# Performance work log

Measured on AMD Instinct MI355X. Metric: run time of the kernel, lower is better.

The kernel has to match this reference:

```python
import jax, jax.numpy as jnp
import numpy as np

B, T, D, E, H = 8, 2048, 1024, 8, 256
LN_EPS = 1e-5  # torch.nn.LayerNorm default


def setup_inputs() -> dict:
    key = jax.random.key(0)
    ks = jax.random.split(key, 4)
    return {
        "x": jax.random.normal(ks[0], (B, T, D), dtype=jnp.float32),
        "Wg": jax.random.normal(ks[1], (E, D), dtype=jnp.float32) * 0.02,
        "ln_scale": jnp.ones((E, D), dtype=jnp.float32),
        "ln_bias": jnp.zeros((E, D), dtype=jnp.float32),
        "W1": jax.random.normal(ks[2], (E, D, H), dtype=jnp.float32) * 0.02,
        "b1": jnp.zeros((E, H), dtype=jnp.float32),
        "W2": jax.random.normal(ks[3], (E, H, D), dtype=jnp.float32) * 0.02,
        "b2": jnp.zeros((E, D), dtype=jnp.float32),
    }


def reference(x, Wg, ln_scale, ln_bias, W1, b1, W2, b2):
    Bs, Ts, Ds = x.shape
    xt = x.reshape(Bs * Ts, Ds)                      # [N, D]
    logits = xt @ Wg.T                               # [N, E]
    # softmax is monotone, so argmax(softmax(logits)) == argmax(logits)
    top1 = jnp.argmax(logits, axis=-1)               # [N] int

    # LayerNorm normalization is expert-independent; compute once.
    mu = jnp.mean(xt, axis=-1, keepdims=True)
    var = jnp.mean(jnp.square(xt - mu), axis=-1, keepdims=True)
    xhat = (xt - mu) * jax.lax.rsqrt(var + LN_EPS)   # [N, D]

    n_experts = Wg.shape[0]

    def body(y, p):
        s_e, b_e, w1, bb1, w2, bb2, eid = p
        h = jax.nn.gelu((xhat * s_e + b_e) @ w1 + bb1, approximate=False)  # [N, H]
        out = h @ w2 + bb2                                                  # [N, D]
        mask = (top1 == eid)[:, None].astype(out.dtype)
        return y + mask * out, None

    y0 = jnp.zeros_like(xt)
    y, _ = jax.lax.scan(
        body, y0, (ln_scale, ln_bias, W1, b1, W2, b2, jnp.arange(n_experts))
    )
    # dropout p=0.0 is identity
    return y.reshape(Bs, Ts, Ds)
```

## Files before the change

### kernel.cpp

```cpp
#include <hip/hip_runtime.h>
#include <math.h>

#define N_TOK 16384
#define D_DIM 1024
#define E_NUM 8
#define H_DIM 256
#define LN_EPS 1e-5f

#define BM 128
#define BN1 64
#define BN2 128
#define BKG 64
#define MAXTILES (N_TOK / BM + E_NUM)
#define MP (MAXTILES * BM)

typedef __attribute__((ext_vector_type(8))) short bf16x8;
typedef __attribute__((ext_vector_type(4))) float f32x4;

__device__ __forceinline__ unsigned short f2bf(float f) {
  union { float f; unsigned u; } cv; cv.f = f;
  unsigned u = cv.u;
  u += 0x7fffu + ((u >> 16) & 1u);
  return (unsigned short)(u >> 16);
}

__device__ __forceinline__ void gl_lds16(const void* g, void* l) {
  __builtin_amdgcn_global_load_lds(
      (const __attribute__((address_space(1))) unsigned int*)g,
      (__attribute__((address_space(3))) unsigned int*)l, 16, 0, 0);
}

__device__ __forceinline__ float gelu_exact_fast(float v) {
  float u = fabsf(v) * 0.70710678118654752f;
  float t = 1.0f / (1.0f + 0.3275911f * u);
  float poly = t * (0.254829592f + t * (-0.284496736f + t * (1.421413741f
             + t * (-1.453152027f + t * 1.061405429f))));
  float er = 1.0f - poly * __expf(-u * u);
  er = v >= 0.0f ? er : -er;
  return 0.5f * v * (1.0f + er);
}

template <int CTRL>
__device__ __forceinline__ int dppi(int x) {
  return __builtin_amdgcn_update_dpp(0, x, CTRL, 0xf, 0xf, true);
}
template <int CTRL>
__device__ __forceinline__ double dppd(double x) {
  union { double d; int i[2]; } u; u.d = x;
  u.i[0] = dppi<CTRL>(u.i[0]);
  u.i[1] = dppi<CTRL>(u.i[1]);
  return u.d;
}
template <int CTRL>
__device__ __forceinline__ float dppf(float x) {
  union { float f; int i; } u; u.f = x;
  u.i = dppi<CTRL>(u.i);
  return u.f;
}
template <int IMM>
__device__ __forceinline__ double swzd(double x) {
  union { double d; int i[2]; } u; u.d = x;
  u.i[0] = __builtin_amdgcn_ds_swizzle(u.i[0], IMM);
  u.i[1] = __builtin_amdgcn_ds_swizzle(u.i[1], IMM);
  return u.d;
}
template <int IMM>
__device__ __forceinline__ float swzf(float x) {
  union { float f; int i; } u; u.f = x;
  u.i = __builtin_amdgcn_ds_swizzle(u.i, IMM);
  return u.f;
}

__global__ __launch_bounds__(256) void smoe_gate(
    const float* __restrict__ x, const float* __restrict__ wg,
    const float* __restrict__ ln_s, const float* __restrict__ ln_b,
    unsigned short* __restrict__ xhat, int* __restrict__ eid)
{
  int lane = threadIdx.x & 63, wave = threadIdx.x >> 6;
  int t = blockIdx.x * 4 + wave;

  const float4* x4 = (const float4*)x + (size_t)t * 256;
  float4 v[4];
  float s = 0.f, ss = 0.f;
#pragma unroll
  for (int j = 0; j < 4; j++) {
    v[j] = x4[lane + 64 * j];
    s  += v[j].x + v[j].y + v[j].z + v[j].w;
    ss += v[j].x * v[j].x + v[j].y * v[j].y + v[j].z * v[j].z + v[j].w * v[j].w;
  }
  const float4* wg4 = (const float4*)wg;
  double lg[E_NUM];
#pragma unroll
  for (int e = 0; e < E_NUM; e++) {
    double acc = 0.0;
#pragma unroll
    for (int j = 0; j < 4; j++) {
      float4 w = wg4[e * 256 + lane + 64 * j];
      acc += (double)v[j].x * w.x + (double)v[j].y * w.y
           + (double)v[j].z * w.z + (double)v[j].w * w.w;
    }
    lg[e] = acc;
  }

  double a0, a1, a2, a3;
  {
    double p0 = dppd<0xB1>(lg[0]), p1 = dppd<0xB1>(lg[1]);
    double p2 = dppd<0xB1>(lg[2]), p3 = dppd<0xB1>(lg[3]);
    double p4 = dppd<0xB1>(lg[4]), p5 = dppd<0xB1>(lg[5]);
    double p6 = dppd<0xB1>(lg[6]), p7 = dppd<0xB1>(lg[7]);
    bool b = lane & 1;
    a0 = b ? lg[1] + p1 : lg[0] + p0;
    a1 = b ? lg[3] + p3 : lg[2] + p2;
    a2 = b ? lg[5] + p5 : lg[4] + p4;
    a3 = b ? lg[7] + p7 : lg[6] + p6;
  }
  double c0, c1;
  {
    double q0 = dppd<0x4E>(a0), q1 = dppd<0x4E>(a1);
    double q2 = dppd<0x4E>(a2), q3 = dppd<0x4E>(a3);
    bool b = (lane >> 1) & 1;
    c0 = b ? a1 + q1 : a0 + q0;
    c1 = b ? a3 + q3 : a2 + q2;
  }
  double c;
  {
    double r0 = swzd<0x101F>(c0), r1 = swzd<0x101F>(c1);
    bool b = (lane >> 2) & 1;
    c = b ? c1 + r1 : c0 + r0;
  }
  c += dppd<0x128>(c);
  c += swzd<0x401F>(c);
  c += __shfl_xor(c, 32, 64);

  double val = c; int idx = lane & 7;
  {
    double ov = dppd<0xB1>(val); int oi = dppi<0xB1>(idx);
    if (ov > val || (ov == val && oi < idx)) { val = ov; idx = oi; }
  }
  {
    double ov = dppd<0x4E>(val); int oi = dppi<0x4E>(idx);
    if (ov > val || (ov == val && oi < idx)) { val = ov; idx = oi; }
  }
  {
    double ov = dppd<0x124>(val); int oi = dppi<0x124>(idx);
    if (ov > val || (ov == val && oi < idx)) { val = ov; idx = oi; }
  }
  int best = idx;

  s += dppf<0xB1>(s);   ss += dppf<0xB1>(ss);
  s += dppf<0x4E>(s);   ss += dppf<0x4E>(ss);
  s += dppf<0x141>(s);  ss += dppf<0x141>(ss);
  s += dppf<0x128>(s);  ss += dppf<0x128>(ss);
  s += swzf<0x401F>(s); ss += swzf<0x401F>(ss);
  s += __shfl_xor(s, 32, 64);
  ss += __shfl_xor(ss, 32, 64);

  float mean = s * (1.0f / (float)D_DIM);
  float var  = ss * (1.0f / (float)D_DIM) - mean * mean;
  float rstd = 1.0f / sqrtf(var + LN_EPS);

  if (lane == 0) eid[t] = best;

  const float4* s4 = (const float4*)(ln_s + (size_t)best * D_DIM);
  const float4* b4 = (const float4*)(ln_b + (size_t)best * D_DIM);
  ushort4* xo = (ushort4*)(xhat + (size_t)t * D_DIM);
#pragma unroll
  for (int j = 0; j < 4; j++) {
    float4 sc = s4[lane + 64 * j], bi = b4[lane + 64 * j];
    ushort4 o;
    o.x = f2bf((v[j].x - mean) * rstd * sc.x + bi.x);
    o.y = f2bf((v[j].y - mean) * rstd * sc.y + bi.y);
    o.z = f2bf((v[j].z - mean) * rstd * sc.z + bi.z);
    o.w = f2bf((v[j].w - mean) * rstd * sc.w + bi.w);
    xo[lane + 64 * j] = o;
  }
}

__global__ __launch_bounds__(1024) void smoe_route_cvt(
    const int* __restrict__ eid, int* __restrict__ texp, int* __restrict__ tokp,
    const float* __restrict__ w1, unsigned short* __restrict__ w1t,
    const float* __restrict__ w2, unsigned short* __restrict__ w2t)
{
  if (blockIdx.x != 0) {
    int bid = blockIdx.x - 1;
    const float* in; unsigned short* out; int R, C;
    if (bid < 512) { in = w1; out = w1t; R = D_DIM; C = H_DIM; }
    else           { in = w2; out = w2t; R = H_DIM; C = D_DIM; bid -= 512; }
    int rt = R / 64, ct = C / 64;
    int e = bid / (rt * ct);
    int rem = bid % (rt * ct);
    int r0 = (rem / ct) * 64, c0 = (rem % ct) * 64;
    __shared__ float tile[64][65];
    int tx = threadIdx.x & 63, ty = threadIdx.x >> 6;
    const float* src = in + (size_t)e * R * C;
#pragma unroll
    for (int i = 0; i < 4; i++)
      tile[ty + 16 * i][tx] = src[(size_t)(r0 + ty + 16 * i) * C + c0 + tx];
    __syncthreads();
    unsigned short* dst = out + (size_t)e * R * C;
#pragma unroll
    for (int i = 0; i < 4; i++)
      dst[(size_t)(c0 + ty + 16 * i) * R + r0 + tx] = f2bf(tile[tx][ty + 16 * i]);
    return;
  }

  int tid = threadIdx.x;
  int lane = tid & 63, wave = tid >> 6;

  int cnt[E_NUM] = {};
  int ee[16];
#pragma unroll
  for (int j = 0; j < 16; j++) {
    int e = eid[j * 1024 + tid];
    ee[j] = e;
#pragma unroll
    for (int k = 0; k < E_NUM; k++) cnt[k] += (e == k);
  }
  int inc[E_NUM];
#pragma unroll
  for (int k = 0; k < E_NUM; k++) inc[k] = cnt[k];
#pragma unroll
  for (int m = 1; m < 64; m <<= 1) {
#pragma unroll
    for (int k = 0; k < E_NUM; k++) {
      int o = __shfl_up(inc[k], m, 64);
      if (lane >= m) inc[k] += o;
    }
  }
  __shared__ int wtot[16][E_NUM];
  __shared__ int wbase[16][E_NUM];
  __shared__ int ebase[E_NUM];
  __shared__ int ecnt[E_NUM];
  __shared__ int epad[E_NUM];
  if (lane == 63)
#pragma unroll
    for (int k = 0; k < E_NUM; k++) wtot[wave][k] = inc[k];
  __syncthreads();
  if (tid == 0) {
    int run[E_NUM] = {};
    for (int w = 0; w < 16; w++)
#pragma unroll
      for (int k = 0; k < E_NUM; k++) { wbase[w][k] = run[k]; run[k] += wtot[w][k]; }
    int b = 0, ti = 0;
    for (int k = 0; k < E_NUM; k++) {
      ecnt[k] = run[k];
      ebase[k] = b;
      int nt = (run[k] + BM - 1) / BM;
      for (int j = 0; j < nt; j++) texp[ti++] = k;
      epad[k] = nt * BM;
      b += nt * BM;
    }
    for (; ti < MAXTILES; ti++) texp[ti] = -1;
  }
  __syncthreads();
  int tb[E_NUM];
#pragma unroll
  for (int k = 0; k < E_NUM; k++) tb[k] = wbase[wave][k] + inc[k] - cnt[k];
  int run2[E_NUM] = {};
#pragma unroll
  for (int j = 0; j < 16; j++) {
    int e = ee[j];
    int r = 0;
#pragma unroll
    for (int k = 0; k < E_NUM; k++) {
      if (e == k) r = tb[k] + run2[k];
      run2[k] += (e == k);
    }
    tokp[ebase[e] + r] = j * 1024 + tid;
  }
#pragma unroll
  for (int k = 0; k < E_NUM; k++) {
    int s0 = ebase[k] + ecnt[k], n = epad[k] - ecnt[k];
    for (int i = tid; i < n; i += 1024) tokp[s0 + i] = -1;
  }
}

__global__ __launch_bounds__(256) void smoe_gemm1(
    const unsigned short* __restrict__ xhat,
    const unsigned short* __restrict__ w1t,
    const float* __restrict__ b1,
    const int* __restrict__ texp,
    const int* __restrict__ tokp,
    unsigned short* __restrict__ hbuf)
{
  int mt = blockIdx.x;
  int e = texp[mt];
  if (e < 0) return;
  int nt = blockIdx.y;
  int tid = threadIdx.x;
  __shared__ unsigned short As[2][BM * BKG];
  __shared__ unsigned short Bs[2][BN1 * BKG];

  int r8 = tid >> 3;
  int c8 = tid & 7;
  int slot = c8 ^ (r8 & 7);

  const unsigned short* asrc[4];
#pragma unroll
  for (int j = 0; j < 4; j++) {
    int row = r8 + 32 * j;
    int tok = tokp[mt * BM + row];
    tok = tok < 0 ? 0 : tok;
    asrc[j] = xhat + (size_t)tok * D_DIM + slot * 8;
  }
  const unsigned short* bsrc[2];
#pragma unroll
  for (int j = 0; j < 2; j++)
    bsrc[j] = w1t + (size_t)e * H_DIM * D_DIM
            + (size_t)(nt * BN1 + r8 + 32 * j) * D_DIM + slot * 8;

  int wave = tid >> 6, lane = tid & 63;
  int wr = (wave >> 1) * 64;
  int wc = (wave & 1) * 32;
  int qm = lane & 15, quad = lane >> 4;

  int arow[4], brow[2], soff[2];
#pragma unroll
  for (int mi = 0; mi < 4; mi++) arow[mi] = (wr + mi * 16 + qm) * BKG;
#pragma unroll
  for (int ni = 0; ni < 2; ni++) brow[ni] = (wc + ni * 16 + qm) * BKG;
#pragma unroll
  for (int kk = 0; kk < 2; kk++) soff[kk] = ((kk * 4 + quad) ^ (qm & 7)) * 8;

  f32x4 acc[4][2] = {};
  int cur = 0;

#pragma unroll
  for (int j = 0; j < 4; j++) gl_lds16(asrc[j], &As[0][j * 2048 + tid * 8]);
#pragma unroll
  for (int j = 0; j < 2; j++) gl_lds16(bsrc[j], &Bs[0][j * 2048 + tid * 8]);
  __syncthreads();

  for (int t = 0; t < D_DIM / BKG; ++t) {
    if (t + 1 < D_DIM / BKG) {
      int k0 = (t + 1) * BKG;
      int nb = cur ^ 1;
#pragma unroll
      for (int j = 0; j < 4; j++) gl_lds16(asrc[j] + k0, &As[nb][j * 2048 + tid * 8]);
#pragma unroll
      for (int j = 0; j < 2; j++) gl_lds16(bsrc[j] + k0, &Bs[nb][j * 2048 + tid * 8]);
    }
    bf16x8 af[2][4], bfr[2][2];
#pragma unroll
    for (int kk = 0; kk < 2; kk++) {
#pragma unroll
      for (int mi = 0; mi < 4; mi++)
        af[kk][mi] = *(const bf16x8*)&As[cur][arow[mi] + soff[kk]];
#pragma unroll
      for (int ni = 0; ni < 2; ni++)
        bfr[kk][ni] = *(const bf16x8*)&Bs[cur][brow[ni] + soff[kk]];
    }
#pragma unroll
    for (int kk = 0; kk < 2; kk++)
#pragma unroll
      for (int mi = 0; mi < 4; mi++)
#pragma unroll
        for (int ni = 0; ni < 2; ni++)
          acc[mi][ni] = __builtin_amdgcn_mfma_f32_16x16x32_bf16(
              af[kk][mi], bfr[kk][ni], acc[mi][ni], 0, 0, 0);
    __syncthreads();
    cur ^= 1;
  }

  int mbase = mt * BM;
#pragma unroll
  for (int ni = 0; ni < 2; ni++) {
    int col = nt * BN1 + wc + ni * 16 + qm;
    float bias = b1[e * H_DIM + col];
#pragma unroll
    for (int mi = 0; mi < 4; mi++) {
      int rl = wr + mi * 16 + quad * 4;
#pragma unroll
      for (int i = 0; i < 4; i++) {
        float g = gelu_exact_fast(acc[mi][ni][i] + bias);
        hbuf[(size_t)(mbase + rl + i) * H_DIM + col] = f2bf(g);
      }
    }
  }
}

__global__ __launch_bounds__(256) void smoe_gemm2(
    const unsigned short* __restrict__ hbuf,
    const unsigned short* __restrict__ w2t,
    const float* __restrict__ b2,
    const int* __restrict__ texp,
    const int* __restrict__ tokp,
    float* __restrict__ y)
{
  int mt = blockIdx.x;
  int e = texp[mt];
  if (e < 0) return;
  int nt = blockIdx.y;
  int tid = threadIdx.x;
  __shared__ unsigned short As[2][BM * BKG];
  __shared__ unsigned short Bs[2][BN2 * BKG];

  int r8 = tid >> 3;
  int c8 = tid & 7;
  int slot = c8 ^ (r8 & 7);

  const unsigned short* asrc[4];
#pragma unroll
  for (int j = 0; j < 4; j++)
    asrc[j] = hbuf + (size_t)(mt * BM + r8 + 32 * j) * H_DIM + slot * 8;
  const unsigned short* bsrc[4];
#pragma unroll
  for (int j = 0; j < 4; j++)
    bsrc[j] = w2t + (size_t)e * D_DIM * H_DIM
            + (size_t)(nt * BN2 + r8 + 32 * j) * H_DIM + slot * 8;

  int wave = tid >> 6, lane = tid & 63;
  int wr = (wave >> 1) * 64;
  int wc = (wave & 1) * 64;
  int qm = lane & 15, quad = lane >> 4;

  int arow[4], brow[4], soff[2];
#pragma unroll
  for (int mi = 0; mi < 4; mi++) arow[mi] = (wr + mi * 16 + qm) * BKG;
#pragma unroll
  for (int ni = 0; ni < 4; ni++) brow[ni] = (wc + ni * 16 + qm) * BKG;
#pragma unroll
  for (int kk = 0; kk < 2; kk++) soff[kk] = ((kk * 4 + quad) ^ (qm & 7)) * 8;

  f32x4 acc[4][4] = {};
  int cur = 0;

#pragma unroll
  for (int j = 0; j < 4; j++) gl_lds16(asrc[j], &As[0][j * 2048 + tid * 8]);
#pragma unroll
  for (int j = 0; j < 4; j++) gl_lds16(bsrc[j], &Bs[0][j * 2048 + tid * 8]);
  __syncthreads();

  for (int t = 0; t < H_DIM / BKG; ++t) {
    if (t + 1 < H_DIM / BKG) {
      int k0 = (t + 1) * BKG;
      int nb = cur ^ 1;
#pragma unroll
      for (int j = 0; j < 4; j++) gl_lds16(asrc[j] + k0, &As[nb][j * 2048 + tid * 8]);
#pragma unroll
      for (int j = 0; j < 4; j++) gl_lds16(bsrc[j] + k0, &Bs[nb][j * 2048 + tid * 8]);
    }
    bf16x8 af[2][4], bfr[2][4];
#pragma unroll
    for (int kk = 0; kk < 2; kk++) {
#pragma unroll
      for (int mi = 0; mi < 4; mi++)
        af[kk][mi] = *(const bf16x8*)&As[cur][arow[mi] + soff[kk]];
#pragma unroll
      for (int ni = 0; ni < 4; ni++)
        bfr[kk][ni] = *(const bf16x8*)&Bs[cur][brow[ni] + soff[kk]];
    }
#pragma unroll
    for (int kk = 0; kk < 2; kk++)
#pragma unroll
      for (int mi = 0; mi < 4; mi++)
#pragma unroll
        for (int ni = 0; ni < 4; ni++)
          acc[mi][ni] = __builtin_amdgcn_mfma_f32_16x16x32_bf16(
              af[kk][mi], bfr[kk][ni], acc[mi][ni], 0, 0, 0);
    __syncthreads();
    cur ^= 1;
  }

  int mbase = mt * BM;
#pragma unroll
  for (int mi = 0; mi < 4; mi++) {
#pragma unroll
    for (int i = 0; i < 4; i++) {
      int row = mbase + wr + mi * 16 + quad * 4 + i;
      int tok = tokp[row];
      if (tok < 0) continue;
#pragma unroll
      for (int ni = 0; ni < 4; ni++) {
        int col = nt * BN2 + wc + ni * 16 + qm;
        y[(size_t)tok * D_DIM + col] = acc[mi][ni][i] + b2[e * D_DIM + col];
      }
    }
  }
}

extern "C" void kernel_launch(void* const* d_in, const int* in_sizes, int n_in,
                              void* d_out, int out_size, void* d_ws, size_t ws_size,
                              hipStream_t stream) {
  (void)in_sizes; (void)n_in; (void)out_size; (void)ws_size;
  const float* x    = (const float*)d_in[0];
  const float* wg   = (const float*)d_in[1];
  const float* ln_s = (const float*)d_in[2];
  const float* ln_b = (const float*)d_in[3];
  const float* w1   = (const float*)d_in[4];
  const float* b1   = (const float*)d_in[5];
  const float* w2   = (const float*)d_in[6];
  const float* b2   = (const float*)d_in[7];
  float* y = (float*)d_out;

  char* ws = (char*)d_ws;
  size_t off = 0;
  auto alloc = [&](size_t bytes) {
    void* p = ws + off;
    off = (off + bytes + 255) & ~(size_t)255;
    return p;
  };
  unsigned short* xhat = (unsigned short*)alloc((size_t)N_TOK * D_DIM * 2);
  unsigned short* w1t  = (unsigned short*)alloc((size_t)E_NUM * D_DIM * H_DIM * 2);
  unsigned short* w2t  = (unsigned short*)alloc((size_t)E_NUM * D_DIM * H_DIM * 2);
  unsigned short* hbuf = (unsigned short*)alloc((size_t)MP * H_DIM * 2);
  int* eid    = (int*)alloc((size_t)N_TOK * 4);
  int* tokp   = (int*)alloc((size_t)MP * 4);
  int* texp   = (int*)alloc((size_t)MAXTILES * 4);

  smoe_gate<<<N_TOK / 4, 256, 0, stream>>>(x, wg, ln_s, ln_b, xhat, eid);
  smoe_route_cvt<<<1025, 1024, 0, stream>>>(eid, texp, tokp, w1, w1t, w2, w2t);
  smoe_gemm1<<<dim3(MAXTILES, H_DIM / BN1), 256, 0, stream>>>(xhat, w1t, b1, texp, tokp, hbuf);
  smoe_gemm2<<<dim3(MAXTILES, D_DIM / BN2), 256, 0, stream>>>(hbuf, w2t, b2, texp, tokp, y);
}
```

Baseline: 243.3 us.

## Replace single-block routing scan with atomic wave-aggregated scatter across many blocks

The serial single-block prefix-scan routing (1024 threads walking all 16K tokens) is replaced by 64 blocks that use ballot-aggregated atomicAdd on per-expert counters to scatter token ids into per-expert lists. The GEMMs derive each tile's expert and offset from the counts instead of a precomputed tile table, and mask padded rows by count. This is meant to remove the latency of the single routing block, which sits on the critical path alongside the weight conversion. The weight-transpose blocks move to 256 threads with more rows each. Token order within an expert becomes nondeterministic, and a memset launch is added.

```diff
diff --git a/kernel.cpp b/kernel.cpp
--- a/kernel.cpp
+++ b/kernel.cpp
@@ -13,6 +13,7 @@
 #define BKG 64
 #define MAXTILES (N_TOK / BM + E_NUM)
 #define MP (MAXTILES * BM)
+#define CSTRIDE 16
 
 typedef __attribute__((ext_vector_type(8))) short bf16x8;
 typedef __attribute__((ext_vector_type(4))) float f32x4;
@@ -176,102 +177,62 @@
   }
 }
 
-__global__ __launch_bounds__(1024) void smoe_route_cvt(
-    const int* __restrict__ eid, int* __restrict__ texp, int* __restrict__ tokp,
+__global__ __launch_bounds__(256) void smoe_scatter_cvt(
+    const int* __restrict__ eid, int* __restrict__ cnt, int* __restrict__ tokp,
     const float* __restrict__ w1, unsigned short* __restrict__ w1t,
     const float* __restrict__ w2, unsigned short* __restrict__ w2t)
 {
-  if (blockIdx.x != 0) {
-    int bid = blockIdx.x - 1;
-    const float* in; unsigned short* out; int R, C;
-    if (bid < 512) { in = w1; out = w1t; R = D_DIM; C = H_DIM; }
-    else           { in = w2; out = w2t; R = H_DIM; C = D_DIM; bid -= 512; }
-    int rt = R / 64, ct = C / 64;
-    int e = bid / (rt * ct);
-    int rem = bid % (rt * ct);
-    int r0 = (rem / ct) * 64, c0 = (rem % ct) * 64;
-    __shared__ float tile[64][65];
-    int tx = threadIdx.x & 63, ty = threadIdx.x >> 6;
-    const float* src = in + (size_t)e * R * C;
-#pragma unroll
-    for (int i = 0; i < 4; i++)
-      tile[ty + 16 * i][tx] = src[(size_t)(r0 + ty + 16 * i) * C + c0 + tx];
-    __syncthreads();
-    unsigned short* dst = out + (size_t)e * R * C;
-#pragma unroll
-    for (int i = 0; i < 4; i++)
-      dst[(size_t)(c0 + ty + 16 * i) * R + r0 + tx] = f2bf(tile[tx][ty + 16 * i]);
+  if (blockIdx.x < 64) {
+    int t = blockIdx.x * 256 + threadIdx.x;
+    int lane = threadIdx.x & 63;
+    int e = eid[t];
+    int pos = 0;
+#pragma unroll
+    for (int k = 0; k < E_NUM; k++) {
+      bool me = (e == k);
+      unsigned long long m = __ballot(me);
+      if (m == 0ull) continue;
+      int leader = __ffsll((unsigned long long)m) - 1;
+      int cw = __popcll(m);
+      int base = 0;
+      if (lane == leader) base = atomicAdd(&cnt[k * CSTRIDE], cw);
+      base = __shfl(base, leader, 64);
+      if (me) pos = base + __popcll(m & ((1ull << lane) - 1ull));
+    }
+    tokp[e * N_TOK + pos] = t;
     return;
   }
 
-  int tid = threadIdx.x;
-  int lane = tid & 63, wave = tid >> 6;
-
-  int cnt[E_NUM] = {};
-  int ee[16];
-#pragma unroll
-  for (int j = 0; j < 16; j++) {
-    int e = eid[j * 1024 + tid];
-    ee[j] = e;
-#pragma unroll
-    for (int k = 0; k < E_NUM; k++) cnt[k] += (e == k);
-  }
-  int inc[E_NUM];
-#pragma unroll
-  for (int k = 0; k < E_NUM; k++) inc[k] = cnt[k];
-#pragma unroll
-  for (int m = 1; m < 64; m <<= 1) {
-#pragma unroll
-    for (int k = 0; k < E_NUM; k++) {
-      int o = __shfl_up(inc[k], m, 64);
-      if (lane >= m) inc[k] += o;
-    }
-  }
-  __shared__ int wtot[16][E_NUM];
-  __shared__ int wbase[16][E_NUM];
-  __shared__ int ebase[E_NUM];
-  __shared__ int ecnt[E_NUM];
-  __shared__ int epad[E_NUM];
-  if (lane == 63)
-#pragma unroll
-    for (int k = 0; k < E_NUM; k++) wtot[wave][k] = inc[k];
+  int bid = blockIdx.x - 64;
+  const float* in; unsigned short* out; int R, C;
+  if (bid < 512) { in = w1; out = w1t; R = D_DIM; C = H_DIM; }
+  else           { in = w2; out = w2t; R = H_DIM; C = D_DIM; bid -= 512; }
+  int rt = R / 64, ct = C / 64;
+  int e = bid / (rt * ct);
+  int rem = bid % (rt * ct);
+  int r0 = (rem / ct) * 64, c0 = (rem % ct) * 64;
+  __shared__ float tile[64][65];
+  int tx = threadIdx.x & 63, ty = threadIdx.x >> 6;
+  const float* src = in + (size_t)e * R * C;
+#pragma unroll
+  for (int i = 0; i < 16; i++)
+    tile[ty + 4 * i][tx] = src[(size_t)(r0 + ty + 4 * i) * C + c0 + tx];
   __syncthreads();
-  if (tid == 0) {
-    int run[E_NUM] = {};
-    for (int w = 0; w < 16; w++)
-#pragma unroll
-      for (int k = 0; k < E_NUM; k++) { wbase[w][k] = run[k]; run[k] += wtot[w][k]; }
-    int b = 0, ti = 0;
-    for (int k = 0; k < E_NUM; k++) {
-      ecnt[k] = run[k];
-      ebase[k] = b;
-      int nt = (run[k] + BM - 1) / BM;
-      for (int j = 0; j < nt; j++) texp[ti++] = k;
-      epad[k] = nt * BM;
-      b += nt * BM;
-    }
-    for (; ti < MAXTILES; ti++) texp[ti] = -1;
-  }
-  __syncthreads();
-  int tb[E_NUM];
-#pragma unroll
-  for (int k = 0; k < E_NUM; k++) tb[k] = wbase[wave][k] + inc[k] - cnt[k];
-  int run2[E_NUM] = {};
-#pragma unroll
-  for (int j = 0; j < 16; j++) {
-    int e = ee[j];
-    int r = 0;
-#pragma unroll
-    for (int k = 0; k < E_NUM; k++) {
-      if (e == k) r = tb[k] + run2[k];
-      run2[k] += (e == k);
-    }
-    tokp[ebase[e] + r] = j * 1024 + tid;
-  }
+  unsigned short* dst = out + (size_t)e * R * C;
+#pragma unroll
+  for (int i = 0; i < 16; i++)
+    dst[(size_t)(c0 + ty + 4 * i) * R + r0 + tx] = f2bf(tile[tx][ty + 4 * i]);
+}
+
+__device__ __forceinline__ void tile_map(const int* __restrict__ cnt, int mt,
+                                         int& e, int& loc, int& ccnt) {
+  int tb = 0; e = 0; loc = -1; ccnt = 0;
 #pragma unroll
   for (int k = 0; k < E_NUM; k++) {
-    int s0 = ebase[k] + ecnt[k], n = epad[k] - ecnt[k];
-    for (int i = tid; i < n; i += 1024) tokp[s0 + i] = -1;
+    int ck = cnt[k * CSTRIDE];
+    int ntk = (ck + BM - 1) >> 7;
+    if (mt >= tb && mt < tb + ntk) { e = k; loc = (mt - tb) * BM; ccnt = ck; }
+    tb += ntk;
   }
 }
 
@@ -279,13 +240,14 @@
     const unsigned short* __restrict__ xhat,
     const unsigned short* __restrict__ w1t,
     const float* __restrict__ b1,
-    const int* __restrict__ texp,
+    const int* __restrict__ cnt,
     const int* __restrict__ tokp,
     unsigned short* __restrict__ hbuf)
 {
   int mt = blockIdx.x;
-  int e = texp[mt];
-  if (e < 0) return;
+  int e, loc, ccnt;
+  tile_map(cnt, mt, e, loc, ccnt);
+  if (loc < 0) return;
   int nt = blockIdx.y;
   int tid = threadIdx.x;
   __shared__ unsigned short As[2][BM * BKG];
@@ -298,9 +260,8 @@
   const unsigned short* asrc[4];
 #pragma unroll
   for (int j = 0; j < 4; j++) {
-    int row = r8 + 32 * j;
-    int tok = tokp[mt * BM + row];
-    tok = tok < 0 ? 0 : tok;
+    int rl = loc + r8 + 32 * j;
+    int tok = rl < ccnt ? tokp[e * N_TOK + rl] : 0;
     asrc[j] = xhat + (size_t)tok * D_DIM + slot * 8;
   }
   const unsigned short* bsrc[2];
@@ -383,13 +344,14 @@
     const unsigned short* __restrict__ hbuf,
     const unsigned short* __restrict__ w2t,
     const float* __restrict__ b2,
-    const int* __restrict__ texp,
+    const int* __restrict__ cnt,
     const int* __restrict__ tokp,
     float* __restrict__ y)
 {
   int mt = blockIdx.x;
-  int e = texp[mt];
-  if (e < 0) return;
+  int e, loc, ccnt;
+  tile_map(cnt, mt, e, loc, ccnt);
+  if (loc < 0) return;
   int nt = blockIdx.y;
   int tid = threadIdx.x;
   __shared__ unsigned short As[2][BM * BKG];
@@ -462,14 +424,13 @@
     cur ^= 1;
   }
 
-  int mbase = mt * BM;
 #pragma unroll
   for (int mi = 0; mi < 4; mi++) {
 #pragma unroll
     for (int i = 0; i < 4; i++) {
-      int row = mbase + wr + mi * 16 + quad * 4 + i;
-      int tok = tokp[row];
-      if (tok < 0) continue;
+      int rl = loc + wr + mi * 16 + quad * 4 + i;
+      if (rl >= ccnt) continue;
+      int tok = tokp[e * N_TOK + rl];
 #pragma unroll
       for (int ni = 0; ni < 4; ni++) {
         int col = nt * BN2 + wc + ni * 16 + qm;
@@ -505,11 +466,12 @@
   unsigned short* w2t  = (unsigned short*)alloc((size_t)E_NUM * D_DIM * H_DIM * 2);
   unsigned short* hbuf = (unsigned short*)alloc((size_t)MP * H_DIM * 2);
   int* eid    = (int*)alloc((size_t)N_TOK * 4);
-  int* tokp   = (int*)alloc((size_t)MP * 4);
-  int* texp   = (int*)alloc((size_t)MAXTILES * 4);
-
+  int* tokp   = (int*)alloc((size_t)E_NUM * N_TOK * 4);
+  int* cnt    = (int*)alloc((size_t)E_NUM * CSTRIDE * 4);
+
+  hipMemsetAsync(cnt, 0, (size_t)E_NUM * CSTRIDE * 4, stream);
   smoe_gate<<<N_TOK / 4, 256, 0, stream>>>(x, wg, ln_s, ln_b, xhat, eid);
-  smoe_route_cvt<<<1025, 1024, 0, stream>>>(eid, texp, tokp, w1, w1t, w2, w2t);
-  smoe_gemm1<<<dim3(MAXTILES, H_DIM / BN1), 256, 0, stream>>>(xhat, w1t, b1, texp, tokp, hbuf);
-  smoe_gemm2<<<dim3(MAXTILES, D_DIM / BN2), 256, 0, stream>>>(hbuf, w2t, b2, texp, tokp, y);
-}
+  smoe_scatter_cvt<<<64 + 1024, 256, 0, stream>>>(eid, cnt, tokp, w1, w1t, w2, w2t);
+  smoe_gemm1<<<dim3(MAXTILES, H_DIM / BN1), 256, 0, stream>>>(xhat, w1t, b1, cnt, tokp, hbuf);
+  smoe_gemm2<<<dim3(MAXTILES, D_DIM / BN2), 256, 0, stream>>>(hbuf, w2t, b2, cnt, tokp, y);
+}
```

Result: faster. 218.1 us (-10.4%).
